# Kernel optimization log

Hardware: AMD Instinct MI355X
Metric: run time of the kernel (lower is better)

The kernel has to match this reference:

```python
import jax, jax.numpy as jnp
import numpy as np

BATCH = 16
D_MODEL = 384
STATE = 64          # state_dim
D_INNER = 384       # ssd_expand * d_model
H = 64
W = 64


def setup_inputs() -> dict:
    key = jax.random.key(0)
    ks = jax.random.split(key, 6)
    x = jax.random.normal(ks[0], (BATCH, D_MODEL, H * W), jnp.float32)
    # 1x1 Conv1d weights stored as 2D matrices [out_ch, in_ch]
    W_bcdt = jax.random.normal(ks[1], (3 * STATE, D_MODEL), jnp.float32) / np.sqrt(D_MODEL).astype(np.float32)
    # depthwise 3x3 conv, groups = 3*STATE -> kernel [3S, 1, 3, 3]
    W_dw = jax.random.normal(ks[2], (3 * STATE, 1, 3, 3), jnp.float32) / 3.0
    W_hz = jax.random.normal(ks[3], (2 * D_INNER, D_MODEL), jnp.float32) / np.sqrt(D_MODEL).astype(np.float32)
    W_out = jax.random.normal(ks[4], (D_MODEL, D_INNER), jnp.float32) / np.sqrt(D_INNER).astype(np.float32)
    A_param = jax.random.uniform(ks[5], (STATE,), jnp.float32, 1.0, 16.0)
    D_param = jnp.ones((1,), jnp.float32)
    return {"x": x, "W_bcdt": W_bcdt, "W_dw": W_dw, "W_hz": W_hz,
            "W_out": W_out, "A_param": A_param, "D_param": D_param,
            "size_h": H, "size_w": W}


def reference(x, W_bcdt, W_dw, W_hz, W_out, A_param, D_param, size_h, size_w):
    b, d, L = x.shape
    S = A_param.shape[0]
    # BCdt_proj: 1x1 conv1d == matmul over channel dim -> [b, 3S, L]
    bcdt = jnp.einsum('od,bdl->bol', W_bcdt, x)
    # depthwise 3x3 conv over the spatial view [b, 3S, H, W]
    xhw = bcdt.reshape(b, 3 * S, size_h, size_w)
    xhw = jax.lax.conv_general_dilated(
        xhw, W_dw, window_strides=(1, 1), padding='SAME',
        dimension_numbers=('NCHW', 'OIHW', 'NCHW'),
        feature_group_count=3 * S)
    bcdt = xhw.reshape(b, 3 * S, L)
    Bm, Cm, dt = jnp.split(bcdt, 3, axis=1)          # each [b, S, L]
    # softmax over the sequence dim with learned A offset
    A = jax.nn.softmax(dt + A_param[None, :, None], axis=-1)
    AB = A * Bm                                       # [b, S, L]
    h = jnp.einsum('bdl,bsl->bds', x, AB)             # x @ AB^T -> [b, d, S]
    hz = jnp.einsum('od,bds->bos', W_hz, h)           # hz_proj -> [b, 2*d_inner, S]
    h1, z = jnp.split(hz, 2, axis=1)                  # each [b, d_inner, S]
    hgate = h1 * jax.nn.silu(z) + h1 * D_param[0]
    hout = jnp.einsum('oe,bes->bos', W_out, hgate)    # out_proj -> [b, d, S]
    y = jnp.einsum('bds,bsl->bdl', hout, Cm)          # h @ C -> [b, d, L]
    y = y.reshape(b, d, size_h, size_w)
    return (y, hout)
```

## Files before the change

kernel.cpp:

```cpp
#include <hip/hip_runtime.h>

typedef unsigned short u16;
typedef short s16x8 __attribute__((ext_vector_type(8)));
typedef float f32x4 __attribute__((ext_vector_type(4)));

#define NB 16
#define DMODEL 384
#define SDIM 64
#define LSEQ 4096
#define C3S 192

__device__ __forceinline__ float b2f(u16 u) {
    union { unsigned int i; float f; } v; v.i = ((unsigned int)u) << 16; return v.f;
}
__device__ __forceinline__ u16 f2b(float f) {
    union { float ff; unsigned int i; } v; v.ff = f;
    unsigned int x = v.i;
    unsigned int r = (x + 0x7fffu + ((x >> 16) & 1u)) >> 16;
    return (u16)r;
}

__global__ __launch_bounds__(256) void k01_mfma(const float* __restrict__ x,
                                                const float* __restrict__ Wb,
                                                u16* __restrict__ rawb) {
    __shared__ __align__(16) u16  XR[32 * 72];
    __shared__ __align__(16) short Bs[64 * 40];
    const int t = threadIdx.x;
    const int l0 = blockIdx.x * 64;
    const int b = blockIdx.y;
    const int lane = t & 63;
    const int w = t >> 6;
    const int lm = lane & 15, kg = lane >> 4;

    f32x4 acc[3][4];
    #pragma unroll
    for (int i = 0; i < 3; ++i)
        #pragma unroll
        for (int j = 0; j < 4; ++j) acc[i][j] = (f32x4){0.f, 0.f, 0.f, 0.f};

    const int xr = t >> 3;
    const int xli = (t & 7) * 8;
    const int bl = t & 63;
    const int bdq = (t >> 6) * 8;

    for (int kc = 0; kc < DMODEL; kc += 32) {
        {
            const float* xp = x + ((size_t)(b * DMODEL + kc + xr)) * LSEQ + l0 + xli;
            float4 x0 = *reinterpret_cast<const float4*>(xp);
            float4 x1 = *reinterpret_cast<const float4*>(xp + 4);
            s16x8 v;
            v[0] = (short)f2b(x0.x); v[1] = (short)f2b(x0.y); v[2] = (short)f2b(x0.z); v[3] = (short)f2b(x0.w);
            v[4] = (short)f2b(x1.x); v[5] = (short)f2b(x1.y); v[6] = (short)f2b(x1.z); v[7] = (short)f2b(x1.w);
            *reinterpret_cast<s16x8*>(&XR[xr * 72 + xli]) = v;
        }
        s16x8 af[3];
        #pragma unroll
        for (int i = 0; i < 3; ++i) {
            const float* wp = Wb + (size_t)(w * 48 + i * 16 + lm) * DMODEL + kc + kg * 8;
            float4 w0 = *reinterpret_cast<const float4*>(wp);
            float4 w1 = *reinterpret_cast<const float4*>(wp + 4);
            af[i][0] = (short)f2b(w0.x); af[i][1] = (short)f2b(w0.y);
            af[i][2] = (short)f2b(w0.z); af[i][3] = (short)f2b(w0.w);
            af[i][4] = (short)f2b(w1.x); af[i][5] = (short)f2b(w1.y);
            af[i][6] = (short)f2b(w1.z); af[i][7] = (short)f2b(w1.w);
        }
        __syncthreads();
        {
            s16x8 v;
            #pragma unroll
            for (int j = 0; j < 8; ++j) v[j] = (short)XR[(bdq + j) * 72 + bl];
            *reinterpret_cast<s16x8*>(&Bs[bl * 40 + bdq]) = v;
        }
        __syncthreads();
        s16x8 bf[4];
        #pragma unroll
        for (int j = 0; j < 4; ++j)
            bf[j] = *reinterpret_cast<s16x8*>(&Bs[(j * 16 + lm) * 40 + kg * 8]);
        #pragma unroll
        for (int i = 0; i < 3; ++i)
            #pragma unroll
            for (int j = 0; j < 4; ++j)
                acc[i][j] = __builtin_amdgcn_mfma_f32_16x16x32_bf16(af[i], bf[j], acc[i][j], 0, 0, 0);
        __syncthreads();
    }
    #pragma unroll
    for (int i = 0; i < 3; ++i) {
        #pragma unroll
        for (int j = 0; j < 4; ++j) {
            #pragma unroll
            for (int r = 0; r < 4; ++r) {
                int o = w * 48 + i * 16 + kg * 4 + r;
                int l = l0 + j * 16 + lm;
                rawb[((size_t)b * C3S + o) * LSEQ + l] = f2b(acc[i][j][r]);
            }
        }
    }
}

__global__ __launch_bounds__(256) void k23_ab(const u16* __restrict__ rawb,
                                              const float* __restrict__ Wdw,
                                              const float* __restrict__ Ap,
                                              u16* __restrict__ AB,
                                              u16* __restrict__ CMB) {
    __shared__ __align__(16) u16 chB[LSEQ];
    __shared__ __align__(16) u16 chC[LSEQ];
    __shared__ __align__(16) u16 chT[LSEQ];
    __shared__ float red[4];
    const int t = threadIdx.x;
    const int s = blockIdx.x;
    const int b = blockIdx.y;
    const u16* rB = rawb + ((size_t)b * C3S + s) * LSEQ;
    const u16* rC = rawb + ((size_t)b * C3S + 64 + s) * LSEQ;
    const u16* rT = rawb + ((size_t)b * C3S + 128 + s) * LSEQ;
    #pragma unroll
    for (int i = 0; i < 2; ++i) {
        int c8 = (t + i * 256) * 8;
        *reinterpret_cast<s16x8*>(&chB[c8]) = *reinterpret_cast<const s16x8*>(rB + c8);
        *reinterpret_cast<s16x8*>(&chC[c8]) = *reinterpret_cast<const s16x8*>(rC + c8);
        *reinterpret_cast<s16x8*>(&chT[c8]) = *reinterpret_cast<const s16x8*>(rT + c8);
    }
    __syncthreads();
    float wB[9], wC[9], wT[9];
    #pragma unroll
    for (int k = 0; k < 9; ++k) {
        wB[k] = Wdw[s * 9 + k];
        wC[k] = Wdw[(64 + s) * 9 + k];
        wT[k] = Wdw[(128 + s) * 9 + k];
    }
    const float a = Ap[s];
    u16* cmp = CMB + ((size_t)b * SDIM + s) * LSEQ;
    float vB[16], vT[16];
    float m = -3.0e38f;
    #pragma unroll
    for (int i = 0; i < 16; ++i) {
        int idx = t + i * 256;
        int row = idx >> 6, col = idx & 63;
        float aB = 0.f, aC = 0.f, aT = 0.f;
        #pragma unroll
        for (int dy = -1; dy <= 1; ++dy) {
            int r = row + dy;
            if (r < 0 || r > 63) continue;
            #pragma unroll
            for (int dx = -1; dx <= 1; ++dx) {
                int cc = col + dx;
                if (cc < 0 || cc > 63) continue;
                int p = r * 64 + cc;
                int wi = (dy + 1) * 3 + (dx + 1);
                aB = fmaf(wB[wi], b2f(chB[p]), aB);
                aC = fmaf(wC[wi], b2f(chC[p]), aC);
                aT = fmaf(wT[wi], b2f(chT[p]), aT);
            }
        }
        cmp[idx] = f2b(aC);
        vB[i] = aB;
        vT[i] = aT + a;
        m = fmaxf(m, vT[i]);
    }
    #pragma unroll
    for (int off = 32; off; off >>= 1) m = fmaxf(m, __shfl_xor(m, off));
    if ((t & 63) == 0) red[t >> 6] = m;
    __syncthreads();
    m = fmaxf(fmaxf(red[0], red[1]), fmaxf(red[2], red[3]));
    __syncthreads();
    float sum = 0.f;
    #pragma unroll
    for (int i = 0; i < 16; ++i) {
        vT[i] = expf(vT[i] - m);
        sum += vT[i];
    }
    #pragma unroll
    for (int off = 32; off; off >>= 1) sum += __shfl_xor(sum, off);
    if ((t & 63) == 0) red[t >> 6] = sum;
    __syncthreads();
    sum = red[0] + red[1] + red[2] + red[3];
    const float inv = 1.0f / sum;
    u16* op = AB + ((size_t)b * SDIM + s) * LSEQ;
    #pragma unroll
    for (int i = 0; i < 16; ++i) {
        int idx = t + i * 256;
        op[idx] = f2b(vT[i] * inv * vB[i]);
    }
}

__global__ __launch_bounds__(256) void kcmT(const u16* __restrict__ CMB,
                                            u16* __restrict__ CmT) {
    __shared__ __align__(16) u16 T[64][72];
    const int t = threadIdx.x;
    const int l0 = blockIdx.x * 64;
    const int b = blockIdx.y;
    const int sr = t >> 2;
    const int lo = (t & 3) * 16;
    const u16* ip = CMB + ((size_t)(b * SDIM + sr)) * LSEQ + l0 + lo;
    s16x8 va = *reinterpret_cast<const s16x8*>(ip);
    s16x8 vb = *reinterpret_cast<const s16x8*>(ip + 8);
    *reinterpret_cast<s16x8*>(&T[sr][lo + 0]) = va;
    *reinterpret_cast<s16x8*>(&T[sr][lo + 8]) = vb;
    __syncthreads();
    const int lr = t >> 2;
    const int sof = (t & 3) * 16;
    s16x8 wa, wb;
    #pragma unroll
    for (int j = 0; j < 8; ++j) {
        wa[j] = (short)T[sof + j][lr];
        wb[j] = (short)T[sof + 8 + j][lr];
    }
    u16* op = CmT + ((size_t)(b * LSEQ + l0 + lr)) * SDIM + sof;
    *reinterpret_cast<s16x8*>(op + 0) = wa;
    *reinterpret_cast<s16x8*>(op + 8) = wb;
}

__global__ __launch_bounds__(256) void k4_mfma(const float* __restrict__ x,
                                               const u16* __restrict__ ABu,
                                               float* __restrict__ hpart) {
    __shared__ __align__(16) short As[32 * 40];
    __shared__ __align__(16) short Bs[64 * 40];
    const int t = threadIdx.x;
    const int d0 = blockIdx.x * 32;
    const int kc = blockIdx.y;
    const int b = blockIdx.z;
    const int lane = t & 63;
    const int w = t >> 6;
    const int wm = w >> 1, wn = w & 1;
    const int lm = lane & 15, kg = lane >> 4;
    const int arow = t >> 2;
    const int aoff = (t & 3) * 8;
    const float* ap = x + ((size_t)(b * DMODEL + d0 + (arow & 31))) * LSEQ + kc * 1024 + aoff;
    const u16* bp = ABu + ((size_t)(b * SDIM + arow)) * LSEQ + kc * 1024 + aoff;
    f32x4 acc[2];
    acc[0] = (f32x4){0.f, 0.f, 0.f, 0.f};
    acc[1] = (f32x4){0.f, 0.f, 0.f, 0.f};

    for (int ks = 0; ks < 1024; ks += 32) {
        if (t < 128) {
            float4 a0 = *reinterpret_cast<const float4*>(ap + ks);
            float4 a1 = *reinterpret_cast<const float4*>(ap + ks + 4);
            s16x8 av;
            av[0] = (short)f2b(a0.x); av[1] = (short)f2b(a0.y); av[2] = (short)f2b(a0.z); av[3] = (short)f2b(a0.w);
            av[4] = (short)f2b(a1.x); av[5] = (short)f2b(a1.y); av[6] = (short)f2b(a1.z); av[7] = (short)f2b(a1.w);
            *reinterpret_cast<s16x8*>(&As[arow * 40 + aoff]) = av;
        }
        s16x8 bv = *reinterpret_cast<const s16x8*>(bp + ks);
        *reinterpret_cast<s16x8*>(&Bs[arow * 40 + aoff]) = bv;
        __syncthreads();
        s16x8 af = *reinterpret_cast<s16x8*>(&As[(wm * 16 + lm) * 40 + kg * 8]);
        s16x8 bf0 = *reinterpret_cast<s16x8*>(&Bs[(wn * 32 + lm) * 40 + kg * 8]);
        s16x8 bf1 = *reinterpret_cast<s16x8*>(&Bs[(wn * 32 + 16 + lm) * 40 + kg * 8]);
        acc[0] = __builtin_amdgcn_mfma_f32_16x16x32_bf16(af, bf0, acc[0], 0, 0, 0);
        acc[1] = __builtin_amdgcn_mfma_f32_16x16x32_bf16(af, bf1, acc[1], 0, 0, 0);
        __syncthreads();
    }
    #pragma unroll
    for (int j = 0; j < 2; ++j) {
        int d = d0 + wm * 16 + kg * 4;
        int s = wn * 32 + j * 16 + lm;
        float* p = hpart + (size_t)kc * (1024 * DMODEL) + ((size_t)b * 64 + s) * DMODEL + d;
        *reinterpret_cast<f32x4*>(p) = acc[j];
    }
}

__global__ __launch_bounds__(256) void k5hz(const float* __restrict__ HPART,
                                            const float* __restrict__ Whz,
                                            float* __restrict__ HZT) {
    __shared__ __align__(16) short As[64 * 40];
    __shared__ __align__(16) short Bs[64 * 40];
    const int t = threadIdx.x;
    const int m0 = blockIdx.x * 64;
    const int n0 = blockIdx.y * 64;
    const int lane = t & 63;
    const int w = t >> 6;
    const int wm = w >> 1, wn = w & 1;
    const int lm = lane & 15, kg = lane >> 4;
    const int arow = t >> 2;
    const int aoff = (t & 3) * 8;
    const int NPART = 1024 * DMODEL;
    const float* apg = HPART + (size_t)(m0 + arow) * DMODEL + aoff;
    const float* bpg = Whz + (size_t)(n0 + arow) * DMODEL + aoff;
    f32x4 acc[2][2];
    #pragma unroll
    for (int i = 0; i < 2; ++i)
        #pragma unroll
        for (int j = 0; j < 2; ++j) acc[i][j] = (f32x4){0.f, 0.f, 0.f, 0.f};

    for (int kc = 0; kc < DMODEL; kc += 32) {
        float4 s0 = make_float4(0.f, 0.f, 0.f, 0.f);
        float4 s1 = make_float4(0.f, 0.f, 0.f, 0.f);
        #pragma unroll
        for (int p = 0; p < 4; ++p) {
            float4 u0 = *reinterpret_cast<const float4*>(apg + (size_t)p * NPART + kc);
            float4 u1 = *reinterpret_cast<const float4*>(apg + (size_t)p * NPART + kc + 4);
            s0.x += u0.x; s0.y += u0.y; s0.z += u0.z; s0.w += u0.w;
            s1.x += u1.x; s1.y += u1.y; s1.z += u1.z; s1.w += u1.w;
        }
        s16x8 av;
        av[0] = (short)f2b(s0.x); av[1] = (short)f2b(s0.y); av[2] = (short)f2b(s0.z); av[3] = (short)f2b(s0.w);
        av[4] = (short)f2b(s1.x); av[5] = (short)f2b(s1.y); av[6] = (short)f2b(s1.z); av[7] = (short)f2b(s1.w);
        float4 b0 = *reinterpret_cast<const float4*>(bpg + kc);
        float4 b1 = *reinterpret_cast<const float4*>(bpg + kc + 4);
        s16x8 bv;
        bv[0] = (short)f2b(b0.x); bv[1] = (short)f2b(b0.y); bv[2] = (short)f2b(b0.z); bv[3] = (short)f2b(b0.w);
        bv[4] = (short)f2b(b1.x); bv[5] = (short)f2b(b1.y); bv[6] = (short)f2b(b1.z); bv[7] = (short)f2b(b1.w);
        *reinterpret_cast<s16x8*>(&As[arow * 40 + aoff]) = av;
        *reinterpret_cast<s16x8*>(&Bs[arow * 40 + aoff]) = bv;
        __syncthreads();
        s16x8 af[2], bf[2];
        #pragma unroll
        for (int i = 0; i < 2; ++i) {
            af[i] = *reinterpret_cast<s16x8*>(&As[(wm * 32 + i * 16 + lm) * 40 + kg * 8]);
            bf[i] = *reinterpret_cast<s16x8*>(&Bs[(wn * 32 + i * 16 + lm) * 40 + kg * 8]);
        }
        #pragma unroll
        for (int i = 0; i < 2; ++i)
            #pragma unroll
            for (int j = 0; j < 2; ++j)
                acc[i][j] = __builtin_amdgcn_mfma_f32_16x16x32_bf16(af[i], bf[j], acc[i][j], 0, 0, 0);
        __syncthreads();
    }
    #pragma unroll
    for (int i = 0; i < 2; ++i) {
        #pragma unroll
        for (int j = 0; j < 2; ++j) {
            #pragma unroll
            for (int r = 0; r < 4; ++r) {
                int bs = m0 + wm * 32 + i * 16 + kg * 4 + r;
                int o = n0 + wn * 32 + j * 16 + lm;
                HZT[(size_t)bs * 768 + o] = acc[i][j][r];
            }
        }
    }
}

__global__ __launch_bounds__(256) void k5ho(const float* __restrict__ HZT,
                                            const float* __restrict__ Wout,
                                            const float* __restrict__ Dp,
                                            float* __restrict__ ho,
                                            u16* __restrict__ hob) {
    __shared__ __align__(16) short As[64 * 40];
    __shared__ __align__(16) short Bs[64 * 40];
    const int t = threadIdx.x;
    const int m0 = blockIdx.x * 64;
    const int n0 = blockIdx.y * 64;
    const int lane = t & 63;
    const int w = t >> 6;
    const int wm = w >> 1, wn = w & 1;
    const int lm = lane & 15, kg = lane >> 4;
    const int arow = t >> 2;
    const int aoff = (t & 3) * 8;
    const float* hzp = HZT + (size_t)(m0 + arow) * 768 + aoff;
    const float* bpg = Wout + (size_t)(n0 + arow) * DMODEL + aoff;
    const float Dv = Dp[0];
    f32x4 acc[2][2];
    #pragma unroll
    for (int i = 0; i < 2; ++i)
        #pragma unroll
        for (int j = 0; j < 2; ++j) acc[i][j] = (f32x4){0.f, 0.f, 0.f, 0.f};

    for (int kc = 0; kc < DMODEL; kc += 32) {
        float4 h0 = *reinterpret_cast<const float4*>(hzp + kc);
        float4 h1 = *reinterpret_cast<const float4*>(hzp + kc + 4);
        float4 z0 = *reinterpret_cast<const float4*>(hzp + DMODEL + kc);
        float4 z1 = *reinterpret_cast<const float4*>(hzp + DMODEL + kc + 4);
        s16x8 av;
        av[0] = (short)f2b(h0.x * (z0.x / (1.f + expf(-z0.x)) + Dv));
        av[1] = (short)f2b(h0.y * (z0.y / (1.f + expf(-z0.y)) + Dv));
        av[2] = (short)f2b(h0.z * (z0.z / (1.f + expf(-z0.z)) + Dv));
        av[3] = (short)f2b(h0.w * (z0.w / (1.f + expf(-z0.w)) + Dv));
        av[4] = (short)f2b(h1.x * (z1.x / (1.f + expf(-z1.x)) + Dv));
        av[5] = (short)f2b(h1.y * (z1.y / (1.f + expf(-z1.y)) + Dv));
        av[6] = (short)f2b(h1.z * (z1.z / (1.f + expf(-z1.z)) + Dv));
        av[7] = (short)f2b(h1.w * (z1.w / (1.f + expf(-z1.w)) + Dv));
        float4 b0 = *reinterpret_cast<const float4*>(bpg + kc);
        float4 b1 = *reinterpret_cast<const float4*>(bpg + kc + 4);
        s16x8 bv;
        bv[0] = (short)f2b(b0.x); bv[1] = (short)f2b(b0.y); bv[2] = (short)f2b(b0.z); bv[3] = (short)f2b(b0.w);
        bv[4] = (short)f2b(b1.x); bv[5] = (short)f2b(b1.y); bv[6] = (short)f2b(b1.z); bv[7] = (short)f2b(b1.w);
        *reinterpret_cast<s16x8*>(&As[arow * 40 + aoff]) = av;
        *reinterpret_cast<s16x8*>(&Bs[arow * 40 + aoff]) = bv;
        __syncthreads();
        s16x8 af[2], bf[2];
        #pragma unroll
        for (int i = 0; i < 2; ++i) {
            af[i] = *reinterpret_cast<s16x8*>(&As[(wm * 32 + i * 16 + lm) * 40 + kg * 8]);
            bf[i] = *reinterpret_cast<s16x8*>(&Bs[(wn * 32 + i * 16 + lm) * 40 + kg * 8]);
        }
        #pragma unroll
        for (int i = 0; i < 2; ++i)
            #pragma unroll
            for (int j = 0; j < 2; ++j)
                acc[i][j] = __builtin_amdgcn_mfma_f32_16x16x32_bf16(af[i], bf[j], acc[i][j], 0, 0, 0);
        __syncthreads();
    }
    #pragma unroll
    for (int i = 0; i < 2; ++i) {
        #pragma unroll
        for (int j = 0; j < 2; ++j) {
            int bs = m0 + wm * 32 + i * 16 + kg * 4;
            int b = bs >> 6, s = bs & 63;
            int o = n0 + wn * 32 + j * 16 + lm;
            size_t idx = ((size_t)b * DMODEL + o) * SDIM + s;
            *reinterpret_cast<f32x4*>(ho + idx) = acc[i][j];
            ushort4 u;
            u.x = f2b(acc[i][j][0]); u.y = f2b(acc[i][j][1]);
            u.z = f2b(acc[i][j][2]); u.w = f2b(acc[i][j][3]);
            *reinterpret_cast<ushort4*>(hob + idx) = u;
        }
    }
}

__global__ __launch_bounds__(256) void k6_mfma(const u16* __restrict__ CmT,
                                               const u16* __restrict__ hob,
                                               float* __restrict__ y) {
    const int t = threadIdx.x;
    const int l0 = blockIdx.x * 128;
    const int d0 = blockIdx.y * 128;
    const int b = blockIdx.z;
    const int lane = t & 63;
    const int w = t >> 6;
    const int wm = w >> 1, wn = w & 1;
    const int lm = lane & 15, kg = lane >> 4;
    const u16* hp = hob + (size_t)b * DMODEL * SDIM;
    const u16* cp = CmT + (size_t)b * LSEQ * SDIM;
    s16x8 af[4][2], bf[4][2];
    #pragma unroll
    for (int i = 0; i < 4; ++i)
        #pragma unroll
        for (int ks = 0; ks < 2; ++ks)
            af[i][ks] = *reinterpret_cast<const s16x8*>(
                hp + (size_t)(d0 + wm * 64 + i * 16 + lm) * SDIM + ks * 32 + kg * 8);
    #pragma unroll
    for (int j = 0; j < 4; ++j)
        #pragma unroll
        for (int ks = 0; ks < 2; ++ks)
            bf[j][ks] = *reinterpret_cast<const s16x8*>(
                cp + (size_t)(l0 + wn * 64 + j * 16 + lm) * SDIM + ks * 32 + kg * 8);
    f32x4 acc[4][4];
    #pragma unroll
    for (int i = 0; i < 4; ++i)
        #pragma unroll
        for (int j = 0; j < 4; ++j) acc[i][j] = (f32x4){0.f, 0.f, 0.f, 0.f};
    #pragma unroll
    for (int ks = 0; ks < 2; ++ks)
        #pragma unroll
        for (int i = 0; i < 4; ++i)
            #pragma unroll
            for (int j = 0; j < 4; ++j)
                acc[i][j] = __builtin_amdgcn_mfma_f32_16x16x32_bf16(af[i][ks], bf[j][ks], acc[i][j], 0, 0, 0);
    float* yp = y + (size_t)b * DMODEL * LSEQ;
    #pragma unroll
    for (int i = 0; i < 4; ++i) {
        #pragma unroll
        for (int j = 0; j < 4; ++j) {
            #pragma unroll
            for (int r = 0; r < 4; ++r) {
                int d = d0 + wm * 64 + i * 16 + kg * 4 + r;
                int l = l0 + wn * 64 + j * 16 + lm;
                yp[(size_t)d * LSEQ + l] = acc[i][j][r];
            }
        }
    }
}

extern "C" void kernel_launch(void* const* d_in, const int* in_sizes, int n_in,
                              void* d_out, int out_size, void* d_ws, size_t ws_size,
                              hipStream_t stream) {
    const float* x    = (const float*)d_in[0];
    const float* Wb   = (const float*)d_in[1];
    const float* Wdw  = (const float*)d_in[2];
    const float* Whz  = (const float*)d_in[3];
    const float* Wout = (const float*)d_in[4];
    const float* Ap   = (const float*)d_in[5];
    const float* Dp   = (const float*)d_in[6];

    float* out = (float*)d_out;
    const size_t YSIZE = (size_t)NB * DMODEL * LSEQ;

    u16*   RAWB   = (u16*)out;
    u16*   CMB    = (u16*)(out + 18874368);
    u16*   ABu    = (u16*)(out + 20971520);
    float* HPART  = out;
    float* HZT    = out + 1572864;
    float* HO     = out + YSIZE;
    u16*   CmT    = (u16*)d_ws;
    u16*   HOB    = (u16*)d_ws + 4194304;

    k01_mfma<<<dim3(64, NB), 256, 0, stream>>>(x, Wb, RAWB);
    k23_ab  <<<dim3(SDIM, NB), 256, 0, stream>>>(RAWB, Wdw, Ap, ABu, CMB);
    kcmT    <<<dim3(64, NB), 256, 0, stream>>>(CMB, CmT);
    k4_mfma <<<dim3(12, 4, NB), 256, 0, stream>>>(x, ABu, HPART);
    k5hz    <<<dim3(16, 12), 256, 0, stream>>>(HPART, Whz, HZT);
    k5ho    <<<dim3(16, 6), 256, 0, stream>>>(HZT, Wout, Dp, HO, HOB);
    k6_mfma <<<dim3(32, 3, NB), 256, 0, stream>>>(CmT, HOB, out);
}
```

Before: 153.5 us.

## Double-buffer k01 staging tiles and widen block to 128 columns with 8 waves

The BCdt projection GEMM kernel now processes 128 sequence positions per block with 512 threads arranged as 4x2 waves. XR and Bs shared buffers are double-buffered, so the next x chunk is loaded while the current one is transposed and consumed. This cuts barriers per k-step from three to one. It halves the grid size and raises shared memory per block, which may reduce parallelism or occupancy.

```diff
diff --git a/kernel.cpp b/kernel.cpp
--- a/kernel.cpp
+++ b/kernel.cpp
@@ -20,16 +20,17 @@
     return (u16)r;
 }
 
-__global__ __launch_bounds__(256) void k01_mfma(const float* __restrict__ x,
-                                                const float* __restrict__ Wb,
-                                                u16* __restrict__ rawb) {
-    __shared__ __align__(16) u16  XR[32 * 72];
-    __shared__ __align__(16) short Bs[64 * 40];
-    const int t = threadIdx.x;
-    const int l0 = blockIdx.x * 64;
+__global__ __launch_bounds__(512, 2) void k01_mfma(const float* __restrict__ x,
+                                                   const float* __restrict__ Wb,
+                                                   u16* __restrict__ rawb) {
+    __shared__ __align__(16) u16  XR[2][32 * 136];
+    __shared__ __align__(16) short Bs[2][128 * 40];
+    const int t = threadIdx.x;
+    const int l0 = blockIdx.x * 128;
     const int b = blockIdx.y;
     const int lane = t & 63;
     const int w = t >> 6;
+    const int wm = w >> 1, wn = w & 1;
     const int lm = lane & 15, kg = lane >> 4;
 
     f32x4 acc[3][4];
@@ -38,25 +39,44 @@
         #pragma unroll
         for (int j = 0; j < 4; ++j) acc[i][j] = (f32x4){0.f, 0.f, 0.f, 0.f};
 
-    const int xr = t >> 3;
-    const int xli = (t & 7) * 8;
-    const int bl = t & 63;
-    const int bdq = (t >> 6) * 8;
-
-    for (int kc = 0; kc < DMODEL; kc += 32) {
+    const int xr = t >> 4;
+    const int xli = (t & 15) * 8;
+    const int bl = t & 127;
+    const int bdq = (t >> 7) * 8;
+
+    {
+        const float* xp = x + ((size_t)(b * DMODEL + xr)) * LSEQ + l0 + xli;
+        float4 x0 = *reinterpret_cast<const float4*>(xp);
+        float4 x1 = *reinterpret_cast<const float4*>(xp + 4);
+        s16x8 v;
+        v[0] = (short)f2b(x0.x); v[1] = (short)f2b(x0.y); v[2] = (short)f2b(x0.z); v[3] = (short)f2b(x0.w);
+        v[4] = (short)f2b(x1.x); v[5] = (short)f2b(x1.y); v[6] = (short)f2b(x1.z); v[7] = (short)f2b(x1.w);
+        *reinterpret_cast<s16x8*>(&XR[0][xr * 136 + xli]) = v;
+    }
+    __syncthreads();
+
+    for (int ks = 0; ks < 12; ++ks) {
+        const int p = ks & 1;
+        const int kc = ks * 32;
         {
-            const float* xp = x + ((size_t)(b * DMODEL + kc + xr)) * LSEQ + l0 + xli;
+            s16x8 v;
+            #pragma unroll
+            for (int j = 0; j < 8; ++j) v[j] = (short)XR[p][(bdq + j) * 136 + bl];
+            *reinterpret_cast<s16x8*>(&Bs[p][bl * 40 + bdq]) = v;
+        }
+        if (ks < 11) {
+            const float* xp = x + ((size_t)(b * DMODEL + kc + 32 + xr)) * LSEQ + l0 + xli;
             float4 x0 = *reinterpret_cast<const float4*>(xp);
             float4 x1 = *reinterpret_cast<const float4*>(xp + 4);
             s16x8 v;
             v[0] = (short)f2b(x0.x); v[1] = (short)f2b(x0.y); v[2] = (short)f2b(x0.z); v[3] = (short)f2b(x0.w);
             v[4] = (short)f2b(x1.x); v[5] = (short)f2b(x1.y); v[6] = (short)f2b(x1.z); v[7] = (short)f2b(x1.w);
-            *reinterpret_cast<s16x8*>(&XR[xr * 72 + xli]) = v;
+            *reinterpret_cast<s16x8*>(&XR[p ^ 1][xr * 136 + xli]) = v;
         }
         s16x8 af[3];
         #pragma unroll
         for (int i = 0; i < 3; ++i) {
-            const float* wp = Wb + (size_t)(w * 48 + i * 16 + lm) * DMODEL + kc + kg * 8;
+            const float* wp = Wb + (size_t)(wm * 48 + i * 16 + lm) * DMODEL + kc + kg * 8;
             float4 w0 = *reinterpret_cast<const float4*>(wp);
             float4 w1 = *reinterpret_cast<const float4*>(wp + 4);
             af[i][0] = (short)f2b(w0.x); af[i][1] = (short)f2b(w0.y);
@@ -65,23 +85,15 @@
             af[i][6] = (short)f2b(w1.z); af[i][7] = (short)f2b(w1.w);
         }
         __syncthreads();
-        {
-            s16x8 v;
-            #pragma unroll
-            for (int j = 0; j < 8; ++j) v[j] = (short)XR[(bdq + j) * 72 + bl];
-            *reinterpret_cast<s16x8*>(&Bs[bl * 40 + bdq]) = v;
-        }
-        __syncthreads();
         s16x8 bf[4];
         #pragma unroll
         for (int j = 0; j < 4; ++j)
-            bf[j] = *reinterpret_cast<s16x8*>(&Bs[(j * 16 + lm) * 40 + kg * 8]);
+            bf[j] = *reinterpret_cast<s16x8*>(&Bs[p][(wn * 64 + j * 16 + lm) * 40 + kg * 8]);
         #pragma unroll
         for (int i = 0; i < 3; ++i)
             #pragma unroll
             for (int j = 0; j < 4; ++j)
                 acc[i][j] = __builtin_amdgcn_mfma_f32_16x16x32_bf16(af[i], bf[j], acc[i][j], 0, 0, 0);
-        __syncthreads();
     }
     #pragma unroll
     for (int i = 0; i < 3; ++i) {
@@ -89,8 +101,8 @@
         for (int j = 0; j < 4; ++j) {
             #pragma unroll
             for (int r = 0; r < 4; ++r) {
-                int o = w * 48 + i * 16 + kg * 4 + r;
-                int l = l0 + j * 16 + lm;
+                int o = wm * 48 + i * 16 + kg * 4 + r;
+                int l = l0 + wn * 64 + j * 16 + lm;
                 rawb[((size_t)b * C3S + o) * LSEQ + l] = f2b(acc[i][j][r]);
             }
         }
@@ -482,7 +494,7 @@
     u16*   CmT    = (u16*)d_ws;
     u16*   HOB    = (u16*)d_ws + 4194304;
 
-    k01_mfma<<<dim3(64, NB), 256, 0, stream>>>(x, Wb, RAWB);
+    k01_mfma<<<dim3(32, NB), 512, 0, stream>>>(x, Wb, RAWB);
     k23_ab  <<<dim3(SDIM, NB), 256, 0, stream>>>(RAWB, Wdw, Ap, ABu, CMB);
     kcmT    <<<dim3(64, NB), 256, 0, stream>>>(CMB, CmT);
     k4_mfma <<<dim3(12, 4, NB), 256, 0, stream>>>(x, ABu, HPART);
```

Measured after the change: 155.3 us. Within noise of the previous version (+1.1%).
